# Performance work log

Hardware: AMD Instinct MI355X
Metric: run time of the kernel (lower is better)

The kernel has to match this reference:

```python
import jax, jax.numpy as jnp
import numpy as np

DATA_BITS = 57
SHIFT_BITS = 6
BATCH = 1_000_000


def setup_inputs() -> dict:
    key = jax.random.key(0)
    kx, ks = jax.random.split(key)
    # binary spike bits in {0,1}, stored as float32 (SNN convention)
    X = jax.random.randint(kx, (BATCH, DATA_BITS), 0, 2).astype(jnp.float32)
    shift = jax.random.randint(ks, (BATCH, SHIFT_BITS), 0, 2).astype(jnp.float32)
    return {"X": X, "shift": shift}


def _barrel_shift_right_sticky(X, shift):
    # X: [..., 57] bits, shift: [..., 6] bits (MSB first)
    zeros = jnp.zeros_like(X[..., 0:1])
    current = X
    sticky_accum = zeros
    for layer in range(SHIFT_BITS):
        shift_amt = 2 ** (SHIFT_BITS - 1 - layer)  # 32,16,8,4,2,1 (all <= 57)
        s_bit = shift[..., layer:layer + 1]  # [..., 1]
        # VecORTree over the bits that would be shifted out
        layer_sticky = jnp.max(current[..., DATA_BITS - shift_amt:], axis=-1, keepdims=True)
        # VecMUX(s, layer_sticky, 0) = s * layer_sticky
        layer_sticky_selected = s_bit * layer_sticky
        # VecOR accumulate (binary OR == max for {0,1})
        sticky_accum = jnp.maximum(sticky_accum, layer_sticky_selected)
        # right shift by shift_amt: prepend zeros, drop low bits (shift_amt < 57 always)
        pad = jnp.zeros(current.shape[:-1] + (shift_amt,), dtype=current.dtype)
        shifted = jnp.concatenate([pad, current[..., :-shift_amt]], axis=-1)
        # VecMUX(s, shifted, current)
        current = s_bit * shifted + (1.0 - s_bit) * current
    return current, sticky_accum


def reference(X, shift):
    return _barrel_shift_right_sticky(X, shift)
```

## Files before the change

kernel.cpp:

```cpp
#include <hip/hip_runtime.h>
#include <stdint.h>

#define DATA_BITS 57
#define SHIFT_BITS 6
#define ROWS_PER_BLOCK 256
#define BLOCK 256
#define TILE_FLOATS (ROWS_PER_BLOCK * DATA_BITS)
#define WORDS (TILE_FLOATS / 64)
#define NITER (TILE_FLOATS / BLOCK)
#define STILE_VEC (ROWS_PER_BLOCK * SHIFT_BITS / 4)
#define MASK57 ((1ULL << DATA_BITS) - 1ULL)

typedef float floatx4 __attribute__((ext_vector_type(4)));

__device__ __forceinline__ floatx4 expand(const unsigned long long* masks, int p) {
    int row = p / DATA_BITS;
    int col = p - row * DATA_BITS;
    unsigned long long m = masks[row] >> col;
    if (col > DATA_BITS - 4)
        m |= masks[row + 1] << (DATA_BITS - col);
    uint32_t c = (uint32_t)m;
    floatx4 f;
    f.x = __uint_as_float((0u - (c        & 1u)) & 0x3F800000u);
    f.y = __uint_as_float((0u - ((c >> 1) & 1u)) & 0x3F800000u);
    f.z = __uint_as_float((0u - ((c >> 2) & 1u)) & 0x3F800000u);
    f.w = __uint_as_float((0u - ((c >> 3) & 1u)) & 0x3F800000u);
    return f;
}

__global__ __launch_bounds__(BLOCK, 4) void barrel57_kernel(
    const float* __restrict__ X, const float* __restrict__ S,
    float* __restrict__ outCur, float* __restrict__ outSticky,
    int batch)
{
    __shared__ unsigned long long words[WORDS + 2];
    __shared__ unsigned long long maskOut[ROWS_PER_BLOCK + 2];
    __shared__ float stile[ROWS_PER_BLOCK * SHIFT_BITS];

    const int t    = threadIdx.x;
    const int wave = t >> 6;
    const int lane = t & 63;
    const long long blockRow0 = (long long)blockIdx.x * ROWS_PER_BLOCK;
    const long long xBase = blockRow0 * DATA_BITS;
    const long long sBase = blockRow0 * SHIFT_BITS;
    const bool fullBlock = (blockRow0 + ROWS_PER_BLOCK <= (long long)batch);

    if (t < 2) { words[WORDS + t] = 0ULL; maskOut[ROWS_PER_BLOCK + t] = 0ULL; }

    const float4* Sv = (const float4*)S + (sBase >> 2);

    if (fullBlock) {
        const float* Xp = X + xBase;
        float f[NITER];
        #pragma unroll
        for (int k = 0; k < NITER; ++k) f[k] = Xp[k * BLOCK + t];

        #pragma unroll
        for (int k = 0; k < 2; ++k) {
            int i = t + k * BLOCK;
            if (i < STILE_VEC) *(float4*)&stile[i * 4] = Sv[i];
        }

        #pragma unroll
        for (int k = 0; k < NITER; ++k) {
            unsigned long long bal = __ballot(f[k] != 0.0f);
            if (lane == 0) words[4 * k + wave] = bal;
        }
    } else {
        const long long totalX = (long long)batch * DATA_BITS;
        const long long totalS = (long long)batch * SHIFT_BITS;
        for (int i = t; i < STILE_VEC; i += BLOCK)
            if (sBase + (long long)i * 4 < totalS) *(float4*)&stile[i * 4] = Sv[i];
        for (int k = 0; k < NITER; ++k) {
            long long g = xBase + (long long)k * BLOCK + t;
            float x = (g < totalX) ? X[g] : 0.0f;
            unsigned long long bal = __ballot(x != 0.0f);
            if (lane == 0) words[4 * k + wave] = bal;
        }
    }
    __syncthreads();

    {
        const long long row = blockRow0 + t;
        unsigned long long outm = 0ULL;
        if (row < batch) {
            const int bitpos = t * DATA_BITS;
            const int w0 = bitpos >> 6;
            const int off = bitpos & 63;
            unsigned long long mask = words[w0] >> off;
            if (off) mask |= words[w0 + 1] << (64 - off);
            mask &= MASK57;

            const float* sr = &stile[t * SHIFT_BITS];
            int s = 0;
            #pragma unroll
            for (int l = 0; l < SHIFT_BITS; ++l)
                s |= (int)(sr[l] != 0.0f) << (SHIFT_BITS - 1 - l);

            outm = (mask << s) & MASK57;
            unsigned long long dropped = (s >= DATA_BITS) ? mask : (mask >> (DATA_BITS - s));
            __builtin_nontemporal_store((dropped != 0ULL) ? 1.0f : 0.0f, &outSticky[row]);
        }
        maskOut[t] = outm;
    }
    __syncthreads();

    floatx4* Ov = (floatx4*)outCur + (xBase >> 2);
    if (fullBlock) {
        #pragma unroll
        for (int k = 0; k < NITER / 4; ++k) {
            int i = t + k * BLOCK;
            __builtin_nontemporal_store(expand(maskOut, i * 4), &Ov[i]);
        }
        if (t < (TILE_FLOATS / 4 - (NITER / 4) * BLOCK)) {
            int i = t + (NITER / 4) * BLOCK;
            __builtin_nontemporal_store(expand(maskOut, i * 4), &Ov[i]);
        }
    } else {
        const long long totalX = (long long)batch * DATA_BITS;
        for (int i = t; i < TILE_FLOATS / 4; i += BLOCK)
            if (xBase + (long long)i * 4 < totalX)
                __builtin_nontemporal_store(expand(maskOut, i * 4), &Ov[i]);
    }
}

extern "C" void kernel_launch(void* const* d_in, const int* in_sizes, int n_in,
                              void* d_out, int out_size, void* d_ws, size_t ws_size,
                              hipStream_t stream) {
    const float* X = (const float*)d_in[0];
    const float* S = (const float*)d_in[1];
    const int batch = in_sizes[1] / SHIFT_BITS;
    float* outCur = (float*)d_out;
    float* outSticky = outCur + (long long)batch * DATA_BITS;

    const int grid = (batch + ROWS_PER_BLOCK - 1) / ROWS_PER_BLOCK;
    barrel57_kernel<<<grid, BLOCK, 0, stream>>>(X, S, outCur, outSticky, batch);
}
```

Before: 73.07 us.

## Stage X tile into LDS via global_load_lds and pack bits per row

Replaces per-element register loads plus wave ballots with direct global-to-LDS 16-byte async loads of the whole float tile (57 KB of LDS per block). Each thread then packs its row's 57 bits by reading the exponent bit of each float from LDS. Shift bits are loaded directly per thread from global memory instead of through a shared tile. Launch bounds drop to 2 blocks per CU to fit the larger LDS footprint, which trades occupancy for fewer instructions and wider loads.

```diff
diff --git a/kernel.cpp b/kernel.cpp
--- a/kernel.cpp
+++ b/kernel.cpp
@@ -6,12 +6,18 @@
 #define ROWS_PER_BLOCK 256
 #define BLOCK 256
 #define TILE_FLOATS (ROWS_PER_BLOCK * DATA_BITS)
-#define WORDS (TILE_FLOATS / 64)
-#define NITER (TILE_FLOATS / BLOCK)
-#define STILE_VEC (ROWS_PER_BLOCK * SHIFT_BITS / 4)
+#define TILE_VEC (TILE_FLOATS / 4)
+#define NSTAGE (TILE_VEC / 64)
 #define MASK57 ((1ULL << DATA_BITS) - 1ULL)
 
 typedef float floatx4 __attribute__((ext_vector_type(4)));
+
+__device__ __forceinline__ void gload_lds16(const float4* g, float4* l) {
+    __builtin_amdgcn_global_load_lds(
+        (const __attribute__((address_space(1))) void*)g,
+        (__attribute__((address_space(3))) void*)l,
+        16, 0, 0);
+}
 
 __device__ __forceinline__ floatx4 expand(const unsigned long long* masks, int p) {
     int row = p / DATA_BITS;
@@ -28,74 +34,73 @@
     return f;
 }
 
-__global__ __launch_bounds__(BLOCK, 4) void barrel57_kernel(
+__global__ __launch_bounds__(BLOCK, 2) void barrel57_kernel(
     const float* __restrict__ X, const float* __restrict__ S,
     float* __restrict__ outCur, float* __restrict__ outSticky,
     int batch)
 {
-    __shared__ unsigned long long words[WORDS + 2];
+    __shared__ float tile[TILE_FLOATS];
     __shared__ unsigned long long maskOut[ROWS_PER_BLOCK + 2];
-    __shared__ float stile[ROWS_PER_BLOCK * SHIFT_BITS];
 
     const int t    = threadIdx.x;
     const int wave = t >> 6;
     const int lane = t & 63;
     const long long blockRow0 = (long long)blockIdx.x * ROWS_PER_BLOCK;
     const long long xBase = blockRow0 * DATA_BITS;
-    const long long sBase = blockRow0 * SHIFT_BITS;
-    const bool fullBlock = (blockRow0 + ROWS_PER_BLOCK <= (long long)batch);
+    const long long row   = blockRow0 + t;
+    const bool fullBlock  = (blockRow0 + ROWS_PER_BLOCK <= (long long)batch);
 
-    if (t < 2) { words[WORDS + t] = 0ULL; maskOut[ROWS_PER_BLOCK + t] = 0ULL; }
+    float sv[SHIFT_BITS];
+    if (row < (long long)batch) {
+        const float* sp = S + row * SHIFT_BITS;
+        #pragma unroll
+        for (int l = 0; l < SHIFT_BITS; ++l) sv[l] = sp[l];
+    } else {
+        #pragma unroll
+        for (int l = 0; l < SHIFT_BITS; ++l) sv[l] = 0.0f;
+    }
 
-    const float4* Sv = (const float4*)S + (sBase >> 2);
-
+    float4* tileV = (float4*)tile;
     if (fullBlock) {
-        const float* Xp = X + xBase;
-        float f[NITER];
+        const float4* Xv = (const float4*)X + (xBase >> 2);
         #pragma unroll
-        for (int k = 0; k < NITER; ++k) f[k] = Xp[k * BLOCK + t];
-
-        #pragma unroll
-        for (int k = 0; k < 2; ++k) {
-            int i = t + k * BLOCK;
-            if (i < STILE_VEC) *(float4*)&stile[i * 4] = Sv[i];
-        }
-
-        #pragma unroll
-        for (int k = 0; k < NITER; ++k) {
-            unsigned long long bal = __ballot(f[k] != 0.0f);
-            if (lane == 0) words[4 * k + wave] = bal;
+        for (int j = 0; j < (NSTAGE + 3) / 4; ++j) {
+            int i = wave + 4 * j;
+            if (i < NSTAGE) gload_lds16(Xv + i * 64 + lane, tileV + i * 64);
         }
     } else {
-        const long long totalX = (long long)batch * DATA_BITS;
-        const long long totalS = (long long)batch * SHIFT_BITS;
-        for (int i = t; i < STILE_VEC; i += BLOCK)
-            if (sBase + (long long)i * 4 < totalS) *(float4*)&stile[i * 4] = Sv[i];
-        for (int k = 0; k < NITER; ++k) {
-            long long g = xBase + (long long)k * BLOCK + t;
-            float x = (g < totalX) ? X[g] : 0.0f;
-            unsigned long long bal = __ballot(x != 0.0f);
-            if (lane == 0) words[4 * k + wave] = bal;
+        const long long totalV = (long long)batch * DATA_BITS / 4;
+        const long long vBase  = xBase >> 2;
+        #pragma unroll
+        for (int j = 0; j < (NSTAGE + 3) / 4; ++j) {
+            int i = wave + 4 * j;
+            if (i < NSTAGE) {
+                long long gi = vBase + i * 64 + lane;
+                if (gi >= totalV) gi = totalV - 1;
+                gload_lds16((const float4*)X + gi, tileV + i * 64);
+            }
         }
     }
+    if (t < 2) maskOut[ROWS_PER_BLOCK + t] = 0ULL;
     __syncthreads();
 
     {
-        const long long row = blockRow0 + t;
         unsigned long long outm = 0ULL;
-        if (row < batch) {
-            const int bitpos = t * DATA_BITS;
-            const int w0 = bitpos >> 6;
-            const int off = bitpos & 63;
-            unsigned long long mask = words[w0] >> off;
-            if (off) mask |= words[w0 + 1] << (64 - off);
-            mask &= MASK57;
+        if (row < (long long)batch) {
+            const float* r = &tile[t * DATA_BITS];
+            uint32_t lo = 0u, hi = 0u;
+            #pragma unroll
+            for (int k = 0; k < 32; ++k)
+                lo |= ((__float_as_uint(r[k]) >> 23) & 1u) << k;
+            #pragma unroll
+            for (int k = 32; k < DATA_BITS; ++k)
+                hi |= ((__float_as_uint(r[k]) >> 23) & 1u) << (k - 32);
+            unsigned long long mask = ((unsigned long long)hi << 32) | lo;
 
-            const float* sr = &stile[t * SHIFT_BITS];
             int s = 0;
             #pragma unroll
             for (int l = 0; l < SHIFT_BITS; ++l)
-                s |= (int)(sr[l] != 0.0f) << (SHIFT_BITS - 1 - l);
+                s |= (int)(sv[l] != 0.0f) << (SHIFT_BITS - 1 - l);
 
             outm = (mask << s) & MASK57;
             unsigned long long dropped = (s >= DATA_BITS) ? mask : (mask >> (DATA_BITS - s));
@@ -108,18 +113,19 @@
     floatx4* Ov = (floatx4*)outCur + (xBase >> 2);
     if (fullBlock) {
         #pragma unroll
-        for (int k = 0; k < NITER / 4; ++k) {
+        for (int k = 0; k < TILE_VEC / BLOCK; ++k) {
             int i = t + k * BLOCK;
             __builtin_nontemporal_store(expand(maskOut, i * 4), &Ov[i]);
         }
-        if (t < (TILE_FLOATS / 4 - (NITER / 4) * BLOCK)) {
-            int i = t + (NITER / 4) * BLOCK;
+        if (t < TILE_VEC - (TILE_VEC / BLOCK) * BLOCK) {
+            int i = t + (TILE_VEC / BLOCK) * BLOCK;
             __builtin_nontemporal_store(expand(maskOut, i * 4), &Ov[i]);
         }
     } else {
-        const long long totalX = (long long)batch * DATA_BITS;
-        for (int i = t; i < TILE_FLOATS / 4; i += BLOCK)
-            if (xBase + (long long)i * 4 < totalX)
+        const long long totalV = (long long)batch * DATA_BITS / 4;
+        const long long vBase  = xBase >> 2;
+        for (int i = t; i < TILE_VEC; i += BLOCK)
+            if (vBase + i < totalV)
                 __builtin_nontemporal_store(expand(maskOut, i * 4), &Ov[i]);
     }
 }
```

Result: no change. 72.94 us (-0.2%).
